# Kernel optimization log

Measured on AMD Instinct MI355X. Metric: run time of the kernel, lower is better.

The kernel has to match this reference:

```python
import jax, jax.numpy as jnp
import numpy as np

N_HEADS = 16


def apply_rotary_emb(x, cos, sin):
    # x: [B, H, S, hd]; cos/sin: [S, hd//2] (broadcast over B, H)
    xr = x.reshape(x.shape[:-1] + (-1, 2))
    r, i = xr[..., 0], xr[..., 1]
    a = r * cos - i * sin
    b = i * cos + r * sin
    return jnp.stack([a, b], axis=-1).reshape(x.shape).astype(x.dtype)


def setup_inputs() -> dict:
    key = jax.random.key(0)
    ks = jax.random.split(key, 7)
    B, S, D = 2, 2048, 1024
    hd = D // N_HEADS
    x = jax.random.normal(ks[0], (B, S, D), dtype=jnp.float32)
    freqs_cos = jax.random.uniform(ks[1], (S, hd // 2), dtype=jnp.float32)
    freqs_sin = jax.random.uniform(ks[2], (S, hd // 2), dtype=jnp.float32)
    sc = 1.0 / np.sqrt(D)
    Wq = jax.random.normal(ks[3], (D, D), dtype=jnp.float32) * sc
    Wk = jax.random.normal(ks[4], (D, D), dtype=jnp.float32) * sc
    Wv = jax.random.normal(ks[5], (D, D), dtype=jnp.float32) * sc
    Wo = jax.random.normal(ks[6], (D, D), dtype=jnp.float32) * sc
    return {"x": x, "freqs_cos": freqs_cos, "freqs_sin": freqs_sin,
            "Wq": Wq, "Wk": Wk, "Wv": Wv, "Wo": Wo}


def reference(x, freqs_cos, freqs_sin, Wq, Wk, Wv, Wo):
    B, S, D = x.shape
    H = N_HEADS
    hd = D // H
    # QKV projections (nn.Linear: x @ W.T)
    q = (x @ Wq.T).reshape(B, S, H, hd).transpose(0, 2, 1, 3)
    k = (x @ Wk.T).reshape(B, S, H, hd).transpose(0, 2, 1, 3)
    v = (x @ Wv.T).reshape(B, S, H, hd).transpose(0, 2, 1, 3)
    q = apply_rotary_emb(q, freqs_cos, freqs_sin)
    k = apply_rotary_emb(k, freqs_cos, freqs_sin)
    # causal SDPA (scale = 1/sqrt(head_dim), as in F.scaled_dot_product_attention)
    scores = jnp.einsum("bhqd,bhkd->bhqk", q, k) * (1.0 / np.sqrt(hd))
    causal = jnp.tril(jnp.ones((S, S), dtype=bool))
    scores = jnp.where(causal, scores, -jnp.inf)
    probs = jax.nn.softmax(scores, axis=-1)
    attn_out = jnp.einsum("bhqk,bhkd->bhqd", probs, v)
    attn_cat = attn_out.transpose(0, 2, 1, 3).reshape(B, S, D)
    return attn_cat @ Wo.T
```

## Files before the change

kernel.cpp:

```cpp
#include <hip/hip_runtime.h>
#include <hip/hip_bf16.h>
#include <cstdint>

typedef __attribute__((ext_vector_type(8))) short short8;
typedef __attribute__((ext_vector_type(4))) float f32x4;

#define B_  2
#define S_  2048
#define D_  1024
#define H_  16
#define HD  64

static __device__ __forceinline__ float bf2f(unsigned int u16) {
    union { unsigned int i; float f; } v; v.i = u16 << 16; return v.f;
}
static __device__ __forceinline__ unsigned short f2bf(float f) {
    union { float f; unsigned int i; } v; v.f = f;
    unsigned int r = v.i + 0x7FFFu + ((v.i >> 16) & 1u);
    return (unsigned short)(r >> 16);
}
static __device__ __forceinline__ unsigned pack_bf16(float hi, float lo) {
    union { float f; unsigned u; } h, l;
    h.f = hi; l.f = lo;
    return __builtin_amdgcn_perm(h.u + 0x8000u, l.u + 0x8000u, 0x07060302);
}
static __device__ __forceinline__ void load_lds_16B(const unsigned short* g, unsigned short* l) {
    __builtin_amdgcn_global_load_lds(
        (const __attribute__((address_space(1))) unsigned int*)g,
        (__attribute__((address_space(3))) unsigned int*)l, 16, 0, 0);
}

__global__ void cvt_all(const float* __restrict__ x,
                        const float* __restrict__ w0, const float* __restrict__ w1,
                        const float* __restrict__ w2, const float* __restrict__ w3,
                        unsigned short* __restrict__ xbf,
                        unsigned short* __restrict__ wdst) {
    int bid = blockIdx.x;
    if (bid < 4096) {
        int i = bid * 256 + threadIdx.x;
        float4 f = ((const float4*)x)[i];
        uint2 o;
        o.x = (unsigned int)f2bf(f.x) | ((unsigned int)f2bf(f.y) << 16);
        o.y = (unsigned int)f2bf(f.z) | ((unsigned int)f2bf(f.w) << 16);
        ((uint2*)xbf)[i] = o;
    } else {
        int wb = bid - 4096;
        int wsel = wb >> 10;
        const float* s = wsel == 0 ? w0 : wsel == 1 ? w1 : wsel == 2 ? w2 : w3;
        int i = (wb & 1023) * 256 + threadIdx.x;
        float4 f = ((const float4*)s)[i];
        uint2 o;
        o.x = (unsigned int)f2bf(f.x) | ((unsigned int)f2bf(f.y) << 16);
        o.y = (unsigned int)f2bf(f.z) | ((unsigned int)f2bf(f.w) << 16);
        ((uint2*)wdst)[(size_t)wsel * 262144 + i] = o;
    }
}

__global__ __launch_bounds__(256) void qkv_gemm(
    const unsigned short* __restrict__ xbf,
    const unsigned short* __restrict__ wq,
    const unsigned short* __restrict__ wk,
    const unsigned short* __restrict__ wv,
    const float* __restrict__ fcos,
    const float* __restrict__ fsin,
    unsigned short* __restrict__ qb,
    unsigned short* __restrict__ kb,
    unsigned short* __restrict__ vb)
{
    __shared__ unsigned short pool[2][2][128 * 32];

    const int tid  = threadIdx.x;
    const int w    = tid >> 6, lane = tid & 63;
    const int l15  = lane & 15, quad = lane >> 4;
    const int wrow = (w >> 1) * 64, wcol = (w & 1) * 64;

    const int m0 = blockIdx.x * 128;
    const int nc = blockIdx.y * 128;
    const int sel = nc >> 10;
    const int n0 = nc & 1023;
    const unsigned short* __restrict__ W = sel == 0 ? wq : (sel == 1 ? wk : wv);

    const int lr = lane >> 2, lc = (lane & 3) * 8;
    const unsigned short* ga = xbf + (size_t)(m0 + w * 16 + lr) * 1024 + lc;
    const unsigned short* gb = W   + (size_t)(n0 + w * 16 + lr) * 1024 + lc;

    f32x4 acc[4][4] = {};

    auto STAGE = [&](int k0, int bufi) {
        load_lds_16B(ga + k0,             &pool[bufi][0][(w * 16) * 32]);
        load_lds_16B(ga + 64 * 1024 + k0, &pool[bufi][0][(64 + w * 16) * 32]);
        load_lds_16B(gb + k0,             &pool[bufi][1][(w * 16) * 32]);
        load_lds_16B(gb + 64 * 1024 + k0, &pool[bufi][1][(64 + w * 16) * 32]);
    };

    STAGE(0, 0);
    __syncthreads();

    int cur = 0;
    for (int k0 = 0; k0 < 1024; k0 += 32) {
        if (k0 + 32 < 1024) STAGE(k0 + 32, cur ^ 1);

        short8 a[4], b[4];
#pragma unroll
        for (int i = 0; i < 4; i++)
            a[i] = *(const short8*)&pool[cur][0][(wrow + i * 16 + l15) * 32 + quad * 8];
#pragma unroll
        for (int j = 0; j < 4; j++)
            b[j] = *(const short8*)&pool[cur][1][(wcol + j * 16 + l15) * 32 + quad * 8];
#pragma unroll
        for (int i = 0; i < 4; i++)
#pragma unroll
            for (int j = 0; j < 4; j++)
                acc[i][j] = __builtin_amdgcn_mfma_f32_16x16x32_bf16(a[i], b[j], acc[i][j], 0, 0, 0);

        __syncthreads();
        cur ^= 1;
    }

    if (sel == 2) {
        unsigned short (*Tt)[136] = reinterpret_cast<unsigned short (*)[136]>(&pool[0][0][0]);
        const int bb  = blockIdx.x >> 4;
        const int m0s = (blockIdx.x & 15) * 128;
        const int h0  = n0 >> 6;
        const int nh  = w & 1;
#pragma unroll
        for (int half = 0; half < 2; half++) {
            __syncthreads();
            if (nh == half) {
#pragma unroll
                for (int i = 0; i < 4; i++)
#pragma unroll
                    for (int j = 0; j < 4; j++) {
                        uint2 pk;
                        pk.x = pack_bf16(acc[i][j][1], acc[i][j][0]);
                        pk.y = pack_bf16(acc[i][j][3], acc[i][j][2]);
                        *(uint2*)&Tt[j * 16 + l15][wrow + i * 16 + quad * 4] = pk;
                    }
            }
            __syncthreads();
            const int row = tid >> 2, cq = tid & 3;
            unsigned short* vrow = vb +
                (((size_t)(bb * H_ + h0 + half)) * HD + row) * S_ + m0s + cq * 32;
#pragma unroll
            for (int k = 0; k < 4; k++) {
                short8 v = *(const short8*)&Tt[row][cq * 32 + k * 8];
                *(short8*)(vrow + k * 8) = v;
            }
        }
    } else {
        unsigned short* __restrict__ Out = sel == 0 ? qb : kb;
        const float qsc = (sel == 0) ? 0.125f * 1.44269504f : 1.0f;
        const int odd = l15 & 1;
#pragma unroll
        for (int i = 0; i < 4; i++)
#pragma unroll
            for (int r = 0; r < 4; r++) {
                int m = m0 + wrow + i * 16 + quad * 4 + r;
                int bb = m >> 11, s = m & 2047;
#pragma unroll
                for (int j = 0; j < 4; j++) {
                    int n = n0 + wcol + j * 16 + l15;
                    int h = n >> 6, d = n & 63;
                    int t = d >> 1;
                    float c  = fcos[s * 32 + t];
                    float si = fsin[s * 32 + t];
                    float own = acc[i][j][r];
                    float oth = __shfl_xor(own, 1, 64);
                    float outv = odd ? (own * c + oth * si) : (own * c - oth * si);
                    Out[(((size_t)(bb * H_ + h) * S_) + s) * HD + d] = f2bf(outv * qsc);
                }
            }
    }
}

__global__ __launch_bounds__(256) void out_gemm(
    const unsigned short* __restrict__ A,
    const unsigned short* __restrict__ Bt,
    float* __restrict__ C)
{
    __shared__ unsigned short Apool[2][128 * 32];
    __shared__ unsigned short Bpool[2][64 * 32];

    const int tid  = threadIdx.x;
    const int w    = tid >> 6, lane = tid & 63;
    const int l15  = lane & 15, quad = lane >> 4;
    const int wrow = (w >> 1) * 64, wcol = (w & 1) * 32;

    const int m0 = blockIdx.x * 128;
    const int n0 = blockIdx.y * 64;

    const int lr = lane >> 2, lc = (lane & 3) * 8;
    const unsigned short* ga = A  + (size_t)(m0 + w * 16 + lr) * 1024 + lc;
    const unsigned short* gb = Bt + (size_t)(n0 + w * 16 + lr) * 1024 + lc;

    f32x4 acc[4][2] = {};

    auto STAGE = [&](int k0, int bufi) {
        load_lds_16B(ga + k0,             &Apool[bufi][(w * 16) * 32]);
        load_lds_16B(ga + 64 * 1024 + k0, &Apool[bufi][(64 + w * 16) * 32]);
        load_lds_16B(gb + k0,             &Bpool[bufi][(w * 16) * 32]);
    };

    STAGE(0, 0);
    __syncthreads();

    int cur = 0;
    for (int k0 = 0; k0 < 1024; k0 += 32) {
        if (k0 + 32 < 1024) STAGE(k0 + 32, cur ^ 1);

        short8 a[4], b[2];
#pragma unroll
        for (int i = 0; i < 4; i++)
            a[i] = *(const short8*)&Apool[cur][(wrow + i * 16 + l15) * 32 + quad * 8];
#pragma unroll
        for (int j = 0; j < 2; j++)
            b[j] = *(const short8*)&Bpool[cur][(wcol + j * 16 + l15) * 32 + quad * 8];
#pragma unroll
        for (int i = 0; i < 4; i++)
#pragma unroll
            for (int j = 0; j < 2; j++)
                acc[i][j] = __builtin_amdgcn_mfma_f32_16x16x32_bf16(a[i], b[j], acc[i][j], 0, 0, 0);

        __syncthreads();
        cur ^= 1;
    }

#pragma unroll
    for (int i = 0; i < 4; i++)
#pragma unroll
        for (int r = 0; r < 4; r++) {
            int m = m0 + wrow + i * 16 + quad * 4 + r;
#pragma unroll
            for (int j = 0; j < 2; j++)
                C[(size_t)m * 1024 + n0 + wcol + j * 16 + l15] = acc[i][j][r];
        }
}

__global__ __launch_bounds__(256) void flash_attn_mfma(
    const unsigned short* __restrict__ qb,
    const unsigned short* __restrict__ kb,
    const unsigned short* __restrict__ vT,
    unsigned short* __restrict__ attnc)
{
    __shared__ __attribute__((aligned(1024))) unsigned short Ks[2][2][64][32];
    __shared__ __attribute__((aligned(1024))) unsigned short Vt[64][64];
    __shared__ unsigned short Pls[4][16][72];

    const int bh   = blockIdx.x;
    const int qtb  = blockIdx.y;
    const int jj = qtb & 7, mm = qtb >> 3;
    const int qt = (mm == 0) ? jj : (mm == 1) ? 31 - jj : (mm == 2) ? 8 + jj : 23 - jj;

    const int b    = bh >> 4, h = bh & 15;
    const int tid  = threadIdx.x;
    const int w    = tid >> 6;
    const int lane = tid & 63;
    const int l15  = lane & 15;
    const int quad = lane >> 4;

    const size_t bhS = (size_t)bh * S_;
    const unsigned short* __restrict__ vTb = vT + (size_t)bh * HD * S_;

    short8 qfrag[2];
    {
        const unsigned short* qp = qb + (bhS + qt * 64 + w * 16 + l15) * HD + quad * 8;
        qfrag[0] = *(const short8*)(qp);
        qfrag[1] = *(const short8*)(qp + 32);
    }

    const int ksrow  = lane >> 2;
    const int ksslot = (lane & 3) ^ ((lane >> 3) & 3);
    const int vsrow  = lane >> 3;
    const int vsslot = (lane & 7) ^ vsrow;

    const int ckq = (quad ^ ((l15 >> 1) & 3)) << 4;
    const int s7  = l15 & 7;

    short8 ones;
#pragma unroll
    for (int i = 0; i < 8; i++) ones[i] = (short)0x3F80;

    f32x4 O[4] = {};
    f32x4 Osum = {};
    float mrow = -INFINITY;

    auto STAGE_K = [&](int jt, int bufi) {
        const int j0 = jt * 64;
        const unsigned short* kg = kb + (bhS + j0 + w * 16 + ksrow) * HD + ksslot * 8;
        load_lds_16B(kg,      &Ks[bufi][0][w * 16][0]);
        load_lds_16B(kg + 32, &Ks[bufi][1][w * 16][0]);
    };
    auto STAGE_V = [&](int jt) {
        const int j0 = jt * 64;
        const unsigned short* vg = vTb + (size_t)(w * 16 + vsrow) * S_ + j0 + vsslot * 8;
        load_lds_16B(vg,          &Vt[w * 16][0]);
        load_lds_16B(vg + 8 * S_, &Vt[w * 16 + 8][0]);
    };

    STAGE_K(0, 0);

    for (int jt = 0; jt <= qt; jt++) {
        const int cur = jt & 1;
        asm volatile("s_waitcnt vmcnt(0)" ::: "memory");
        __builtin_amdgcn_s_barrier();

        STAGE_V(jt);
        if (jt < qt) STAGE_K(jt + 1, cur ^ 1);

        const bool diag  = (jt == qt);
        const int  nsub  = diag ? (w + 1) : 4;
        const int  kgmax = (nsub + 1) >> 1;

        f32x4 Sacc[4];
        float tmax = -INFINITY;
        for (int sub = 0; sub < nsub; sub++) {
            f32x4 s = {};
#pragma unroll
            for (int kh = 0; kh < 2; kh++) {
                int bo = ((sub * 16 + l15) << 6) + ckq;
                short8 kf = *(const short8*)((const char*)&Ks[cur][kh][0][0] + bo);
                s = __builtin_amdgcn_mfma_f32_16x16x32_bf16(kf, qfrag[kh], s, 0, 0, 0);
            }
#pragma unroll
            for (int r = 0; r < 4; r++) {
                float v = s[r];
                if (diag && (sub * 16 + quad * 4 + r > w * 16 + l15)) v = -INFINITY;
                s[r] = v;
                tmax = fmaxf(tmax, v);
            }
            Sacc[sub] = s;
        }
        tmax = fmaxf(tmax, __shfl_xor(tmax, 16, 64));
        tmax = fmaxf(tmax, __shfl_xor(tmax, 32, 64));

        if (__any(tmax > mrow + 8.0f)) {
            float mnew = fmaxf(mrow, tmax);
            float ccr  = __builtin_amdgcn_exp2f(mrow - mnew);
#pragma unroll
            for (int r = 0; r < 4; r++) {
                float ccq = __shfl(ccr, quad * 4 + r, 64);
#pragma unroll
                for (int dt = 0; dt < 4; dt++) O[dt][r] *= ccq;
                Osum[r] *= ccq;
            }
            mrow = mnew;
        }

        for (int sub = 0; sub < nsub; sub++) {
            f32x4 s = Sacc[sub];
            float p0 = __builtin_amdgcn_exp2f(s[0] - mrow);
            float p1 = __builtin_amdgcn_exp2f(s[1] - mrow);
            float p2 = __builtin_amdgcn_exp2f(s[2] - mrow);
            float p3 = __builtin_amdgcn_exp2f(s[3] - mrow);
            uint2 pk;
            pk.x = pack_bf16(p1, p0);
            pk.y = pack_bf16(p3, p2);
            *(uint2*)&Pls[w][l15][sub * 16 + quad * 4] = pk;
        }
        if (diag) {
            for (int sub = nsub; sub < 2 * kgmax; sub++) {
                uint2 z; z.x = 0u; z.y = 0u;
                *(uint2*)&Pls[w][l15][sub * 16 + quad * 4] = z;
            }
        }

        if (jt < qt) {
            asm volatile("s_waitcnt vmcnt(2)" ::: "memory");
        } else {
            asm volatile("s_waitcnt vmcnt(0)" ::: "memory");
        }
        __builtin_amdgcn_s_barrier();

        for (int kg = 0; kg < kgmax; kg++) {
            short8 pf = *(const short8*)&Pls[w][l15][kg * 32 + quad * 8];
#pragma unroll
            for (int dt = 0; dt < 4; dt++) {
                int row = dt * 16 + l15;
                int slot = (((kg << 2) | quad) ^ s7) << 4;
                short8 vf = *(const short8*)((const char*)&Vt[0][0] + (row << 7) + slot);
                O[dt] = __builtin_amdgcn_mfma_f32_16x16x32_bf16(pf, vf, O[dt], 0, 0, 0);
            }
            Osum = __builtin_amdgcn_mfma_f32_16x16x32_bf16(pf, ones, Osum, 0, 0, 0);
        }
    }

#pragma unroll
    for (int r = 0; r < 4; r++) {
        float invq = 1.0f / Osum[r];
        int qabs = qt * 64 + w * 16 + quad * 4 + r;
        unsigned short* op = attnc + (((size_t)b * S_ + qabs) * H_ + h) * HD + l15;
#pragma unroll
        for (int dt = 0; dt < 4; dt++)
            op[dt * 16] = f2bf(O[dt][r] * invq);
    }
}

extern "C" void kernel_launch(void* const* d_in, const int* in_sizes, int n_in,
                              void* d_out, int out_size, void* d_ws, size_t ws_size,
                              hipStream_t stream) {
    const float* x    = (const float*)d_in[0];
    const float* fcos = (const float*)d_in[1];
    const float* fsin = (const float*)d_in[2];
    const float* Wq   = (const float*)d_in[3];
    const float* Wk   = (const float*)d_in[4];
    const float* Wv   = (const float*)d_in[5];
    const float* Wo   = (const float*)d_in[6];
    float* out = (float*)d_out;

    unsigned short* ws = (unsigned short*)d_ws;
    unsigned short* xbf = ws;
    unsigned short* wqb = xbf + 4096 * 1024;
    unsigned short* wkb = wqb + 1024 * 1024;
    unsigned short* wvb = wkb + 1024 * 1024;
    unsigned short* wob = wvb + 1024 * 1024;
    unsigned short* qb  = wob + 1024 * 1024;
    unsigned short* kb  = qb + 4096 * 1024;
    unsigned short* vb  = kb + 4096 * 1024;
    unsigned short* attnc = vb + 4096 * 1024;

    cvt_all<<<8192, 256, 0, stream>>>(x, Wq, Wk, Wv, Wo, xbf, wqb);

    qkv_gemm<<<dim3(32, 24), 256, 0, stream>>>(xbf, wqb, wkb, wvb, fcos, fsin, qb, kb, vb);

    flash_attn_mfma<<<dim3(32, 32), 256, 0, stream>>>(qb, kb, vb, attnc);

    out_gemm<<<dim3(32, 16), 256, 0, stream>>>(attnc, wob, out);
}
```

Measured before the change: 208.5 us.

## Deepen out-projection K tile with XOR-swizzled LDS, tidy softmax masking and bf16 packing

```diff
diff --git a/kernel.cpp b/kernel.cpp
--- a/kernel.cpp
+++ b/kernel.cpp
@@ -23,6 +23,11 @@
     union { float f; unsigned u; } h, l;
     h.f = hi; l.f = lo;
     return __builtin_amdgcn_perm(h.u + 0x8000u, l.u + 0x8000u, 0x07060302);
+}
+static __device__ __forceinline__ unsigned cvt_pk_bf16(float a, float b) {
+    unsigned r;
+    asm("v_cvt_pk_bf16_f32 %0, %1, %2" : "=v"(r) : "v"(a), "v"(b));
+    return r;
 }
 static __device__ __forceinline__ void load_lds_16B(const unsigned short* g, unsigned short* l) {
     __builtin_amdgcn_global_load_lds(
@@ -178,8 +183,8 @@
     const unsigned short* __restrict__ Bt,
     float* __restrict__ C)
 {
-    __shared__ unsigned short Apool[2][128 * 32];
-    __shared__ unsigned short Bpool[2][64 * 32];
+    __shared__ __attribute__((aligned(1024))) unsigned short Apool[2][128 * 64];
+    __shared__ __attribute__((aligned(1024))) unsigned short Bpool[2][64 * 64];
 
     const int tid  = threadIdx.x;
     const int w    = tid >> 6, lane = tid & 63;
@@ -189,37 +194,53 @@
     const int m0 = blockIdx.x * 128;
     const int n0 = blockIdx.y * 64;
 
-    const int lr = lane >> 2, lc = (lane & 3) * 8;
-    const unsigned short* ga = A  + (size_t)(m0 + w * 16 + lr) * 1024 + lc;
-    const unsigned short* gb = Bt + (size_t)(n0 + w * 16 + lr) * 1024 + lc;
+    const int srow  = lane >> 3;
+    const int sslot = (lane & 7) ^ srow;
+    const int s7    = l15 & 7;
 
     f32x4 acc[4][2] = {};
 
     auto STAGE = [&](int k0, int bufi) {
-        load_lds_16B(ga + k0,             &Apool[bufi][(w * 16) * 32]);
-        load_lds_16B(ga + 64 * 1024 + k0, &Apool[bufi][(64 + w * 16) * 32]);
-        load_lds_16B(gb + k0,             &Bpool[bufi][(w * 16) * 32]);
+        const unsigned short* gaa = A + (size_t)m0 * 1024 + k0 + sslot * 8;
+        load_lds_16B(gaa + (size_t)(w * 16 + srow) * 1024,          &Apool[bufi][(w * 16) * 64]);
+        load_lds_16B(gaa + (size_t)(w * 16 + 8 + srow) * 1024,      &Apool[bufi][(w * 16 + 8) * 64]);
+        load_lds_16B(gaa + (size_t)(64 + w * 16 + srow) * 1024,     &Apool[bufi][(64 + w * 16) * 64]);
+        load_lds_16B(gaa + (size_t)(64 + w * 16 + 8 + srow) * 1024, &Apool[bufi][(64 + w * 16 + 8) * 64]);
+        const unsigned short* gbb = Bt + (size_t)n0 * 1024 + k0 + sslot * 8;
+        load_lds_16B(gbb + (size_t)(w * 16 + srow) * 1024,          &Bpool[bufi][(w * 16) * 64]);
+        load_lds_16B(gbb + (size_t)(w * 16 + 8 + srow) * 1024,      &Bpool[bufi][(w * 16 + 8) * 64]);
     };
 
     STAGE(0, 0);
     __syncthreads();
 
     int cur = 0;
-    for (int k0 = 0; k0 < 1024; k0 += 32) {
-        if (k0 + 32 < 1024) STAGE(k0 + 32, cur ^ 1);
-
-        short8 a[4], b[2];
-#pragma unroll
-        for (int i = 0; i < 4; i++)
-            a[i] = *(const short8*)&Apool[cur][(wrow + i * 16 + l15) * 32 + quad * 8];
-#pragma unroll
-        for (int j = 0; j < 2; j++)
-            b[j] = *(const short8*)&Bpool[cur][(wcol + j * 16 + l15) * 32 + quad * 8];
-#pragma unroll
-        for (int i = 0; i < 4; i++)
-#pragma unroll
-            for (int j = 0; j < 2; j++)
-                acc[i][j] = __builtin_amdgcn_mfma_f32_16x16x32_bf16(a[i], b[j], acc[i][j], 0, 0, 0);
+    for (int k0 = 0; k0 < 1024; k0 += 64) {
+        if (k0 + 64 < 1024) STAGE(k0 + 64, cur ^ 1);
+
+        short8 a[4][2], b[2][2];
+#pragma unroll
+        for (int kk = 0; kk < 2; kk++) {
+#pragma unroll
+            for (int i = 0; i < 4; i++) {
+                int row = wrow + i * 16 + l15;
+                int slot = (((kk << 2) | quad) ^ s7) << 4;
+                a[i][kk] = *(const short8*)((const char*)&Apool[cur][0] + (row << 7) + slot);
+            }
+#pragma unroll
+            for (int j = 0; j < 2; j++) {
+                int row = wcol + j * 16 + l15;
+                int slot = (((kk << 2) | quad) ^ s7) << 4;
+                b[j][kk] = *(const short8*)((const char*)&Bpool[cur][0] + (row << 7) + slot);
+            }
+        }
+#pragma unroll
+        for (int kk = 0; kk < 2; kk++)
+#pragma unroll
+            for (int i = 0; i < 4; i++)
+#pragma unroll
+                for (int j = 0; j < 2; j++)
+                    acc[i][j] = __builtin_amdgcn_mfma_f32_16x16x32_bf16(a[i][kk], b[j][kk], acc[i][j], 0, 0, 0);
 
         __syncthreads();
         cur ^= 1;
@@ -321,13 +342,13 @@
                 short8 kf = *(const short8*)((const char*)&Ks[cur][kh][0][0] + bo);
                 s = __builtin_amdgcn_mfma_f32_16x16x32_bf16(kf, qfrag[kh], s, 0, 0, 0);
             }
-#pragma unroll
-            for (int r = 0; r < 4; r++) {
-                float v = s[r];
-                if (diag && (sub * 16 + quad * 4 + r > w * 16 + l15)) v = -INFINITY;
-                s[r] = v;
-                tmax = fmaxf(tmax, v);
-            }
+            if (diag) {
+#pragma unroll
+                for (int r = 0; r < 4; r++)
+                    if (sub * 16 + quad * 4 + r > w * 16 + l15) s[r] = -INFINITY;
+            }
+            float sm = fmaxf(fmaxf(s[0], s[1]), fmaxf(s[2], s[3]));
+            tmax = fmaxf(tmax, sm);
             Sacc[sub] = s;
         }
         tmax = fmaxf(tmax, __shfl_xor(tmax, 16, 64));
@@ -353,8 +374,8 @@
             float p2 = __builtin_amdgcn_exp2f(s[2] - mrow);
             float p3 = __builtin_amdgcn_exp2f(s[3] - mrow);
             uint2 pk;
-            pk.x = pack_bf16(p1, p0);
-            pk.y = pack_bf16(p3, p2);
+            pk.x = cvt_pk_bf16(p0, p1);
+            pk.y = cvt_pk_bf16(p2, p3);
             *(uint2*)&Pls[w][l15][sub * 16 + quad * 4] = pk;
         }
         if (diag) {
```

Result: faster. 201.7 us (-3.3%).
